# Performance work log

Measured on AMD Instinct MI355X. Metric: run time of the kernel, lower is better.

## Reference

```python
import jax, jax.numpy as jnp
import numpy as np

B, H, SQ, SK, D = 2, 16, 2048, 2048, 128
P_DROP = 0.5


def setup_inputs() -> dict:
    key = jax.random.key(0)
    kq, kk, kv, km = jax.random.split(key, 4)
    query = jax.random.normal(kq, (B, H, SQ, D), dtype=jnp.float32)
    key_t = jax.random.normal(kk, (B, H, SK, D), dtype=jnp.float32)
    value = jax.random.normal(kv, (B, H, SK, D), dtype=jnp.float32)
    # deterministic Bernoulli(0.5) keep-mask standing in for dropout(p=0.5, train=True)
    dropout_mask = jax.random.randint(km, (B, H, SQ, SK), 0, 2, dtype=jnp.int32)
    return {"query": query, "key": key_t, "value": value, "dropout_mask": dropout_mask}


def reference(query, key, value, dropout_mask):
    d = query.shape[-1]
    # original: scaled_qk = qk.div(d ** -0.5)  ==  qk * sqrt(d)  (faithful to source)
    scale = jnp.asarray(d, query.dtype) ** 0.5
    qk = jnp.einsum("bhqd,bhkd->bhqk", query, key)  # [B,H,SQ,SK]
    scaled_qk = qk * scale
    keep_scale = jnp.asarray(1.0 / (1.0 - P_DROP), query.dtype)
    dropped = jnp.where(dropout_mask == 1, scaled_qk * keep_scale, jnp.zeros((), query.dtype))
    out = jnp.einsum("bhqk,bhkd->bhqd", dropped, value)  # [B,H,SQ,D]
    return out
```

## Files before the change

### kernel.cpp

```cpp
#include <hip/hip_runtime.h>
#include <hip/hip_bf16.h>

#define B_   2
#define H_   16
#define SQ_  2048
#define SK_  2048
#define D_   128

#define QT   128
#define KT   32
#define NITER (SK_/KT)

using bf16x8 = __attribute__((ext_vector_type(8))) __bf16;
using bf16x4 = __attribute__((ext_vector_type(4))) __bf16;
using bf16x2 = __attribute__((ext_vector_type(2))) __bf16;
using f32x4  = __attribute__((ext_vector_type(4))) float;

#define MFMA16(a,b,c) __builtin_amdgcn_mfma_f32_16x16x32_bf16(a,b,c,0,0,0)

#define K_PITCH  136
#define VT_PITCH 40
#define P_PITCH  40
#define M8_PITCH 40

#define KB_   (KT*K_PITCH*2)
#define VTB_  (D_*VT_PITCH*2)
#define M8B_  (QT*M8_PITCH)
#define PSB_  (QT*P_PITCH*2)
#define SMEM_BYTES (2*KB_ + 2*VTB_ + 2*M8B_ + PSB_)

__global__ __launch_bounds__(512, 4)
void attn_drop_kernel(const float* __restrict__ Q,
                      const float* __restrict__ K,
                      const float* __restrict__ V,
                      const int*   __restrict__ M,
                      float* __restrict__ Out)
{
    __shared__ __align__(16) char smem[SMEM_BYTES];
    __bf16* Ps = (__bf16*)(smem + 2*KB_ + 2*VTB_ + 2*M8B_);

    const int tid  = threadIdx.x;
    const int wave = tid >> 6;
    const int lane = tid & 63;
    const int quad = lane >> 4;
    const int ln   = lane & 15;

    const int orig = ((blockIdx.x & 7) << 6) | (blockIdx.x >> 3);
    const int bh = orig >> 4;
    const int qb = orig & 15;

    const float* qptr = Q + ((size_t)bh*SQ_ + (size_t)qb*QT) * D_;
    const float* kptr = K + (size_t)bh*SK_*D_;
    const float* vptr = V + (size_t)bh*SK_*D_;
    const int*   mptr = M + (size_t)bh*(size_t)SQ_*SK_ + (size_t)qb*QT*SK_;
    float*       optr = Out + ((size_t)bh*SQ_ + (size_t)qb*QT) * D_;

    const int c  = tid & 31;
    const int g  = tid >> 5;
    const int mc = tid & 7;
    const int mg = tid >> 3;

    const int wxor = (2*g) ^ ((c & 3) * 8);
    const int vrd  = 8 * (quad ^ ((ln >> 2) & 3));

    float4 kpre0, kpre1, vpre0, vpre1;
    int4   mpre0, mpre1;

    auto load_tile = [&](int kt) {
        const float4* ks = (const float4*)(kptr + (size_t)kt*KT*D_);
        const float4* vs = (const float4*)(vptr + (size_t)kt*KT*D_);
        kpre0 = ks[g*32 + c];
        kpre1 = ks[(g+16)*32 + c];
        vpre0 = vs[(2*g  )*32 + c];
        vpre1 = vs[(2*g+1)*32 + c];
        const int* mrow = mptr + kt*KT + 4*mc;
        mpre0 = *(const int4*)(mrow + (size_t)mg*SK_);
        mpre1 = *(const int4*)(mrow + (size_t)(mg+64)*SK_);
    };

    auto write_tile = [&](int b) {
        __bf16* ksb = (__bf16*)(smem + b*KB_);
        __bf16* vtb = (__bf16*)(smem + 2*KB_ + b*VTB_);
        unsigned char* msb = (unsigned char*)(smem + 2*KB_ + 2*VTB_ + b*M8B_);
        {
            bf16x4 h0 = { (__bf16)kpre0.x, (__bf16)kpre0.y, (__bf16)kpre0.z, (__bf16)kpre0.w };
            bf16x4 h1 = { (__bf16)kpre1.x, (__bf16)kpre1.y, (__bf16)kpre1.z, (__bf16)kpre1.w };
            *(bf16x4*)&ksb[ g      *K_PITCH + 4*c] = h0;
            *(bf16x4*)&ksb[(g+16)  *K_PITCH + 4*c] = h1;
        }
        {
            const float* f0 = (const float*)&vpre0;
            const float* f1 = (const float*)&vpre1;
            #pragma unroll
            for (int j = 0; j < 4; ++j) {
                bf16x2 pr = { (__bf16)f0[j], (__bf16)f1[j] };
                *(bf16x2*)&vtb[(4*c + j)*VT_PITCH + wxor] = pr;
            }
        }
        {
            unsigned pk0 = (unsigned)(mpre0.x & 1) | ((unsigned)(mpre0.y & 1) << 8)
                         | ((unsigned)(mpre0.z & 1) << 16) | ((unsigned)(mpre0.w & 1) << 24);
            unsigned pk1 = (unsigned)(mpre1.x & 1) | ((unsigned)(mpre1.y & 1) << 8)
                         | ((unsigned)(mpre1.z & 1) << 16) | ((unsigned)(mpre1.w & 1) << 24);
            *(unsigned*)&msb[ mg      *M8_PITCH + 4*mc] = pk0;
            *(unsigned*)&msb[(mg+64)  *M8_PITCH + 4*mc] = pk1;
        }
    };

    load_tile(0);

    bf16x8 qf[4];
    {
        const float* qrow = qptr + (size_t)(16*wave + ln)*D_;
        #pragma unroll
        for (int s = 0; s < 4; ++s) {
            float4 a = *(const float4*)(qrow + 32*s + 8*quad);
            float4 b2 = *(const float4*)(qrow + 32*s + 8*quad + 4);
            qf[s] = (bf16x8){ (__bf16)a.x, (__bf16)a.y, (__bf16)a.z, (__bf16)a.w,
                              (__bf16)b2.x, (__bf16)b2.y, (__bf16)b2.z, (__bf16)b2.w };
        }
    }

    f32x4 Oacc[8];
    #pragma unroll
    for (int dt = 0; dt < 8; ++dt)
        Oacc[dt] = (f32x4){0.f, 0.f, 0.f, 0.f};

    const int row0 = 16*wave + 4*quad;

    for (int kt = 0; kt < NITER; ++kt) {
        const int b = kt & 1;
        write_tile(b);
        __syncthreads();
        if (kt + 1 < NITER) load_tile(kt + 1);

        const __bf16* ksb = (const __bf16*)(smem + b*KB_);
        const __bf16* vtb = (const __bf16*)(smem + 2*KB_ + b*VTB_);
        const unsigned char* msb = (const unsigned char*)(smem + 2*KB_ + 2*VTB_ + b*M8B_);

        f32x4 S0 = (f32x4){0.f,0.f,0.f,0.f};
        f32x4 S1 = (f32x4){0.f,0.f,0.f,0.f};
        __builtin_amdgcn_s_setprio(1);
        #pragma unroll
        for (int s = 0; s < 4; ++s) {
            bf16x8 kf0 = *(const bf16x8*)&ksb[ ln      *K_PITCH + 32*s + 8*quad];
            bf16x8 kf1 = *(const bf16x8*)&ksb[(16+ln)  *K_PITCH + 32*s + 8*quad];
            S0 = MFMA16(qf[s], kf0, S0);
            S1 = MFMA16(qf[s], kf1, S1);
        }
        __builtin_amdgcn_s_setprio(0);

        #pragma unroll
        for (int r = 0; r < 4; ++r) {
            float p0 = msb[(row0 + r)*M8_PITCH + ln     ] ? S0[r] : 0.0f;
            float p1 = msb[(row0 + r)*M8_PITCH + 16 + ln] ? S1[r] : 0.0f;
            Ps[(row0 + r)*P_PITCH + ln     ] = (__bf16)p0;
            Ps[(row0 + r)*P_PITCH + 16 + ln] = (__bf16)p1;
        }

        bf16x8 pf = *(const bf16x8*)&Ps[(16*wave + ln)*P_PITCH + 8*quad];
        __builtin_amdgcn_s_setprio(1);
        #pragma unroll
        for (int dt = 0; dt < 8; ++dt) {
            bf16x8 vf = *(const bf16x8*)&vtb[(16*dt + ln)*VT_PITCH + vrd];
            Oacc[dt] = MFMA16(pf, vf, Oacc[dt]);
        }
        __builtin_amdgcn_s_setprio(0);
    }

    const float SCALE = 22.62741699796952f;
    #pragma unroll
    for (int dt = 0; dt < 8; ++dt) {
        #pragma unroll
        for (int r = 0; r < 4; ++r)
            optr[(size_t)(row0 + r)*D_ + 16*dt + ln] = Oacc[dt][r] * SCALE;
    }
}

extern "C" void kernel_launch(void* const* d_in, const int* in_sizes, int n_in,
                              void* d_out, int out_size, void* d_ws, size_t ws_size,
                              hipStream_t stream) {
    (void)in_sizes; (void)n_in; (void)d_ws; (void)ws_size; (void)out_size;
    const float* Q = (const float*)d_in[0];
    const float* K = (const float*)d_in[1];
    const float* V = (const float*)d_in[2];
    const int*   M = (const int*)d_in[3];
    float* Out = (float*)d_out;

    dim3 grid(B_ * H_ * (SQ_ / QT));
    attn_drop_kernel<<<grid, 512, 0, stream>>>(Q, K, V, M, Out);
}
```

Measured before the change: 786.7 us.

## Keep scores in registers by transposing QK MFMA and permuting V reads

Swaps the MFMA operand order for the QK product so each lane holds a transposed score fragment that can feed the PV MFMA directly as its A operand. This removes the LDS round trip for the probability tile and the shared-memory staging of the packed dropout mask. Each lane now loads its own mask values straight from global memory, and V is read as two 4-element halves in a matching permuted k order. The cost is less coalesced mask loads (16-byte per-lane row loads), extra register pressure, and two half-width LDS reads per V fragment.

```diff
diff --git a/kernel.cpp b/kernel.cpp
--- a/kernel.cpp
+++ b/kernel.cpp
@@ -20,14 +20,10 @@
 
 #define K_PITCH  136
 #define VT_PITCH 40
-#define P_PITCH  40
-#define M8_PITCH 40
 
 #define KB_   (KT*K_PITCH*2)
 #define VTB_  (D_*VT_PITCH*2)
-#define M8B_  (QT*M8_PITCH)
-#define PSB_  (QT*P_PITCH*2)
-#define SMEM_BYTES (2*KB_ + 2*VTB_ + 2*M8B_ + PSB_)
+#define SMEM_BYTES (2*KB_ + 2*VTB_)
 
 __global__ __launch_bounds__(512, 4)
 void attn_drop_kernel(const float* __restrict__ Q,
@@ -37,7 +33,6 @@
                       float* __restrict__ Out)
 {
     __shared__ __align__(16) char smem[SMEM_BYTES];
-    __bf16* Ps = (__bf16*)(smem + 2*KB_ + 2*VTB_ + 2*M8B_);
 
     const int tid  = threadIdx.x;
     const int wave = tid >> 6;
@@ -57,36 +52,40 @@
 
     const int c  = tid & 31;
     const int g  = tid >> 5;
-    const int mc = tid & 7;
-    const int mg = tid >> 3;
 
     const int wxor = (2*g) ^ ((c & 3) * 8);
-    const int vrd  = 8 * (quad ^ ((ln >> 2) & 3));
+
+    const int* mlane = mptr + (size_t)(16*wave + ln)*SK_ + 4*quad;
+
+    const int x3  = (ln >> 2) & 3;
+    const int p0c = (quad >> 1) ^ x3;
+    const int vlo = 8*p0c       + 4*(quad & 1);
+    const int vhi = 8*(p0c ^ 2) + 4*(quad & 1);
 
     float4 kpre0, kpre1, vpre0, vpre1;
     int4   mpre0, mpre1;
 
-    auto load_tile = [&](int kt) {
+    auto load_kv = [&](int kt) {
         const float4* ks = (const float4*)(kptr + (size_t)kt*KT*D_);
         const float4* vs = (const float4*)(vptr + (size_t)kt*KT*D_);
         kpre0 = ks[g*32 + c];
         kpre1 = ks[(g+16)*32 + c];
         vpre0 = vs[(2*g  )*32 + c];
         vpre1 = vs[(2*g+1)*32 + c];
-        const int* mrow = mptr + kt*KT + 4*mc;
-        mpre0 = *(const int4*)(mrow + (size_t)mg*SK_);
-        mpre1 = *(const int4*)(mrow + (size_t)(mg+64)*SK_);
+    };
+    auto load_mask = [&](int kt) {
+        mpre0 = *(const int4*)(mlane + kt*KT);
+        mpre1 = *(const int4*)(mlane + kt*KT + 16);
     };
 
     auto write_tile = [&](int b) {
         __bf16* ksb = (__bf16*)(smem + b*KB_);
         __bf16* vtb = (__bf16*)(smem + 2*KB_ + b*VTB_);
-        unsigned char* msb = (unsigned char*)(smem + 2*KB_ + 2*VTB_ + b*M8B_);
         {
             bf16x4 h0 = { (__bf16)kpre0.x, (__bf16)kpre0.y, (__bf16)kpre0.z, (__bf16)kpre0.w };
             bf16x4 h1 = { (__bf16)kpre1.x, (__bf16)kpre1.y, (__bf16)kpre1.z, (__bf16)kpre1.w };
-            *(bf16x4*)&ksb[ g      *K_PITCH + 4*c] = h0;
-            *(bf16x4*)&ksb[(g+16)  *K_PITCH + 4*c] = h1;
+            *(bf16x4*)&ksb[ g    *K_PITCH + 4*c] = h0;
+            *(bf16x4*)&ksb[(g+16)*K_PITCH + 4*c] = h1;
         }
         {
             const float* f0 = (const float*)&vpre0;
@@ -97,26 +96,19 @@
                 *(bf16x2*)&vtb[(4*c + j)*VT_PITCH + wxor] = pr;
             }
         }
-        {
-            unsigned pk0 = (unsigned)(mpre0.x & 1) | ((unsigned)(mpre0.y & 1) << 8)
-                         | ((unsigned)(mpre0.z & 1) << 16) | ((unsigned)(mpre0.w & 1) << 24);
-            unsigned pk1 = (unsigned)(mpre1.x & 1) | ((unsigned)(mpre1.y & 1) << 8)
-                         | ((unsigned)(mpre1.z & 1) << 16) | ((unsigned)(mpre1.w & 1) << 24);
-            *(unsigned*)&msb[ mg      *M8_PITCH + 4*mc] = pk0;
-            *(unsigned*)&msb[(mg+64)  *M8_PITCH + 4*mc] = pk1;
-        }
     };
 
-    load_tile(0);
+    load_kv(0);
+    load_mask(0);
 
     bf16x8 qf[4];
     {
         const float* qrow = qptr + (size_t)(16*wave + ln)*D_;
         #pragma unroll
         for (int s = 0; s < 4; ++s) {
-            float4 a = *(const float4*)(qrow + 32*s + 8*quad);
+            float4 a  = *(const float4*)(qrow + 32*s + 8*quad);
             float4 b2 = *(const float4*)(qrow + 32*s + 8*quad + 4);
-            qf[s] = (bf16x8){ (__bf16)a.x, (__bf16)a.y, (__bf16)a.z, (__bf16)a.w,
+            qf[s] = (bf16x8){ (__bf16)a.x,  (__bf16)a.y,  (__bf16)a.z,  (__bf16)a.w,
                               (__bf16)b2.x, (__bf16)b2.y, (__bf16)b2.z, (__bf16)b2.w };
         }
     }
@@ -132,38 +124,43 @@
         const int b = kt & 1;
         write_tile(b);
         __syncthreads();
-        if (kt + 1 < NITER) load_tile(kt + 1);
+        if (kt + 1 < NITER) load_kv(kt + 1);
 
         const __bf16* ksb = (const __bf16*)(smem + b*KB_);
         const __bf16* vtb = (const __bf16*)(smem + 2*KB_ + b*VTB_);
-        const unsigned char* msb = (const unsigned char*)(smem + 2*KB_ + 2*VTB_ + b*M8B_);
 
         f32x4 S0 = (f32x4){0.f,0.f,0.f,0.f};
         f32x4 S1 = (f32x4){0.f,0.f,0.f,0.f};
         __builtin_amdgcn_s_setprio(1);
         #pragma unroll
         for (int s = 0; s < 4; ++s) {
-            bf16x8 kf0 = *(const bf16x8*)&ksb[ ln      *K_PITCH + 32*s + 8*quad];
-            bf16x8 kf1 = *(const bf16x8*)&ksb[(16+ln)  *K_PITCH + 32*s + 8*quad];
-            S0 = MFMA16(qf[s], kf0, S0);
-            S1 = MFMA16(qf[s], kf1, S1);
+            bf16x8 kf0 = *(const bf16x8*)&ksb[ ln    *K_PITCH + 32*s + 8*quad];
+            bf16x8 kf1 = *(const bf16x8*)&ksb[(16+ln)*K_PITCH + 32*s + 8*quad];
+            S0 = MFMA16(kf0, qf[s], S0);
+            S1 = MFMA16(kf1, qf[s], S1);
         }
         __builtin_amdgcn_s_setprio(0);
 
-        #pragma unroll
-        for (int r = 0; r < 4; ++r) {
-            float p0 = msb[(row0 + r)*M8_PITCH + ln     ] ? S0[r] : 0.0f;
-            float p1 = msb[(row0 + r)*M8_PITCH + 16 + ln] ? S1[r] : 0.0f;
-            Ps[(row0 + r)*P_PITCH + ln     ] = (__bf16)p0;
-            Ps[(row0 + r)*P_PITCH + 16 + ln] = (__bf16)p1;
-        }
+        bf16x8 pa;
+        pa[0] = mpre0.x ? (__bf16)S0[0] : (__bf16)0.0f;
+        pa[1] = mpre0.y ? (__bf16)S0[1] : (__bf16)0.0f;
+        pa[2] = mpre0.z ? (__bf16)S0[2] : (__bf16)0.0f;
+        pa[3] = mpre0.w ? (__bf16)S0[3] : (__bf16)0.0f;
+        pa[4] = mpre1.x ? (__bf16)S1[0] : (__bf16)0.0f;
+        pa[5] = mpre1.y ? (__bf16)S1[1] : (__bf16)0.0f;
+        pa[6] = mpre1.z ? (__bf16)S1[2] : (__bf16)0.0f;
+        pa[7] = mpre1.w ? (__bf16)S1[3] : (__bf16)0.0f;
 
-        bf16x8 pf = *(const bf16x8*)&Ps[(16*wave + ln)*P_PITCH + 8*quad];
+        if (kt + 1 < NITER) load_mask(kt + 1);
+
         __builtin_amdgcn_s_setprio(1);
         #pragma unroll
         for (int dt = 0; dt < 8; ++dt) {
-            bf16x8 vf = *(const bf16x8*)&vtb[(16*dt + ln)*VT_PITCH + vrd];
-            Oacc[dt] = MFMA16(pf, vf, Oacc[dt]);
+            const __bf16* vrow = &vtb[(16*dt + ln)*VT_PITCH];
+            bf16x4 va = *(const bf16x4*)&vrow[vlo];
+            bf16x4 vb = *(const bf16x4*)&vrow[vhi];
+            bf16x8 vf = { va[0], va[1], va[2], va[3], vb[0], vb[1], vb[2], vb[3] };
+            Oacc[dt] = MFMA16(pa, vf, Oacc[dt]);
         }
         __builtin_amdgcn_s_setprio(0);
     }
```

Result: no change. 786.1 us (-0.1%).
